# Kernel tuning notes

Measured on AMD Instinct MI355X. Metric: run time of the kernel, lower is better.

Reference implementation:

```python
import jax, jax.numpy as jnp
import numpy as np

# ----- config (mirrors SpatialAxis init) -----
B, N = 1, 32768
D_MODEL, NHEAD, DEPTH = 256, 8, 2
COORD = 3
PATCH = 512          # self.patch_size default
BITS = 10            # self.morton_bits default
SHIFT = True         # self.shift_order default
MLP_H = 4 * D_MODEL
HD = D_MODEL // NHEAD
EPS = 1e-5


def _part1by2(v):
    # spread low 10 bits of int32 so there are 2 zero bits between each
    v = v & 0x000003FF
    v = (v | (v << 16)) & 0x030000FF
    v = (v | (v << 8)) & 0x0300F00F
    v = (v | (v << 4)) & 0x030C30C3
    v = (v | (v << 2)) & 0x09249249
    return v


def _perm_for_block(coords, i):
    # Z-order (Morton) serialization with per-block axis rotation; odd blocks
    # shift the order by half a patch (shifted-window style). Returns [B,N] int32.
    c = jax.lax.stop_gradient(coords)[..., np.roll(np.arange(COORD), -i)]
    cmin = c.min(axis=1, keepdims=True)
    cmax = c.max(axis=1, keepdims=True)
    q = ((c - cmin) / (cmax - cmin + 1e-9) * (2 ** BITS - 1)).astype(jnp.int32)
    q = jnp.clip(q, 0, 2 ** BITS - 1)
    code = (_part1by2(q[..., 0]) | (_part1by2(q[..., 1]) << 1)
            | (_part1by2(q[..., 2]) << 2))  # [B,N]
    perm = jnp.argsort(code, axis=1)
    if SHIFT and (i % 2 == 1):
        perm = jnp.roll(perm, PATCH // 2, axis=1)
    return perm


def _ln(x, g, b):
    m = x.mean(-1, keepdims=True)
    v = x.var(-1, keepdims=True)
    return (x - m) * jax.lax.rsqrt(v + EPS) * g + b


def _point_block(xs, cs, p):
    # xs: [M, P, D] tokens of one patch each; cs: [M, P, 3]
    M, P, D = xs.shape
    h = _ln(xs, p['ln1_g'], p['ln1_b'])
    qkv = h @ p['w_qkv'] + p['b_qkv']                         # [M,P,3D]
    q, k, v = jnp.split(qkv, 3, axis=-1)
    q = q.reshape(M, P, NHEAD, HD)
    k = k.reshape(M, P, NHEAD, HD)
    v = v.reshape(M, P, NHEAD, HD)
    scores = jnp.einsum('mphd,mqhd->mhpq', q, k) / np.sqrt(HD).astype(np.float32)
    rel = cs[:, :, None, :] - cs[:, None, :, :]               # [M,P,P,3]
    bias = jnp.einsum('mpqc,ch->mhpq', rel, p['w_pos']) + p['b_pos'][None, :, None, None]
    attn = jax.nn.softmax(scores + bias, axis=-1)
    o = jnp.einsum('mhpq,mqhd->mphd', attn, v).reshape(M, P, D)
    xs = xs + o @ p['w_proj'] + p['b_proj']
    h2 = _ln(xs, p['ln2_g'], p['ln2_b'])
    xs = xs + jax.nn.gelu(h2 @ p['w_fc1'] + p['b_fc1']) @ p['w_fc2'] + p['b_fc2']
    return xs


def _forward(x, coords, params):
    Cc = coords.shape[-1]
    nblk = N // PATCH
    for i in range(DEPTH):
        p = {k: v[i] for k, v in params.items()}
        perm = _perm_for_block(coords, i)                      # [B,N]
        inv = jnp.argsort(perm, axis=1)
        x_s = jnp.take_along_axis(x, perm[:, :, None], axis=1)
        c_s = jnp.take_along_axis(coords, perm[:, :, None], axis=1)
        x_f = x_s.reshape(B * nblk, PATCH, D_MODEL)
        c_f = c_s.reshape(B * nblk, PATCH, Cc)
        y = _point_block(x_f, c_f, p).reshape(B, N, D_MODEL)
        x = jnp.take_along_axis(y, inv[:, :, None], axis=1)
    return _ln(x, params['norm_g'][0], params['norm_b'][0])


def setup_inputs() -> dict:
    key = jax.random.key(0)
    ks = jax.random.split(key, 20)
    s = 0.02
    d = {
        'x': jax.random.normal(ks[0], (B, N, D_MODEL), jnp.float32),
        'coords': jax.random.uniform(ks[1], (B, N, COORD), jnp.float32),
        'ln1_g': jnp.ones((DEPTH, D_MODEL), jnp.float32),
        'ln1_b': jnp.zeros((DEPTH, D_MODEL), jnp.float32),
        'w_qkv': jax.random.normal(ks[2], (DEPTH, D_MODEL, 3 * D_MODEL), jnp.float32) * s,
        'b_qkv': jnp.zeros((DEPTH, 3 * D_MODEL), jnp.float32),
        'w_proj': jax.random.normal(ks[3], (DEPTH, D_MODEL, D_MODEL), jnp.float32) * s,
        'b_proj': jnp.zeros((DEPTH, D_MODEL), jnp.float32),
        'w_pos': jax.random.normal(ks[4], (DEPTH, COORD, NHEAD), jnp.float32) * s,
        'b_pos': jnp.zeros((DEPTH, NHEAD), jnp.float32),
        'ln2_g': jnp.ones((DEPTH, D_MODEL), jnp.float32),
        'ln2_b': jnp.zeros((DEPTH, D_MODEL), jnp.float32),
        'w_fc1': jax.random.normal(ks[5], (DEPTH, D_MODEL, MLP_H), jnp.float32) * s,
        'b_fc1': jnp.zeros((DEPTH, MLP_H), jnp.float32),
        'w_fc2': jax.random.normal(ks[6], (DEPTH, MLP_H, D_MODEL), jnp.float32) * s,
        'b_fc2': jnp.zeros((DEPTH, D_MODEL), jnp.float32),
        'norm_g': jnp.ones((1, D_MODEL), jnp.float32),
        'norm_b': jnp.zeros((1, D_MODEL), jnp.float32),
    }
    return d


def reference(x, coords, ln1_g, ln1_b, w_qkv, b_qkv, w_proj, b_proj, w_pos, b_pos,
              ln2_g, ln2_b, w_fc1, b_fc1, w_fc2, b_fc2, norm_g, norm_b):
    params = dict(ln1_g=ln1_g, ln1_b=ln1_b, w_qkv=w_qkv, b_qkv=b_qkv,
                  w_proj=w_proj, b_proj=b_proj, w_pos=w_pos, b_pos=b_pos,
                  ln2_g=ln2_g, ln2_b=ln2_b, w_fc1=w_fc1, b_fc1=b_fc1,
                  w_fc2=w_fc2, b_fc2=b_fc2, norm_g=norm_g, norm_b=norm_b)
    return _forward(x, coords, params)
```

## Files before the change

### kernel.cpp

```cpp
#include <hip/hip_runtime.h>

typedef unsigned long long u64;
typedef unsigned int u32;
typedef unsigned short u16;
typedef float f32x4 __attribute__((ext_vector_type(4)));
typedef __bf16 bf16x8 __attribute__((ext_vector_type(8)));

#define N_TOK 32768

__device__ inline u16 f2bf(float f){
  u32 x = __float_as_uint(f);
  u32 r = x + 0x7FFFu + ((x >> 16) & 1u);
  return (u16)(r >> 16);
}

__device__ inline u16 f2bf_hw(float f){
  u32 pk;
  asm("v_cvt_pk_bf16_f32 %0, %1, %2" : "=v"(pk) : "v"(f), "v"(0.f));
  return (u16)pk;
}

__device__ inline f32x4 mfma16(bf16x8 a, bf16x8 b, f32x4 c){
  return __builtin_amdgcn_mfma_f32_16x16x32_bf16(a, b, c, 0, 0, 0);
}

__device__ inline float fexp2(float x){
  float r;
  asm("v_exp_f32 %0, %1" : "=v"(r) : "v"(x));
  return r;
}
__device__ inline float frcp(float x){
  float r;
  asm("v_rcp_f32 %0, %1" : "=v"(r) : "v"(x));
  return r;
}

typedef const __attribute__((address_space(1))) unsigned int* gas_ptr;
typedef __attribute__((address_space(3))) unsigned int* las_ptr;
__device__ inline void gload_lds16(const u16* g, u16* l){
  __builtin_amdgcn_global_load_lds((gas_ptr)g, (las_ptr)l, 16, 0, 0);
}

__device__ inline u32 rp_idx(const u64* __restrict__ keys, int j, int shift){
  return (u32)(keys[(j + N_TOK - shift) & (N_TOK - 1)] & 0xFFFFull);
}

__device__ inline float gelu_tanh(float x){
  float u = 0.7978845608028654f * (x + 0.044715f * x * x * x);
  float e = fexp2(2.8853900817779268f * u);
  return 0.5f * x * (2.0f - 2.0f * frcp(e + 1.0f));
}

__device__ inline u32 part1by2(u32 v){
  v &= 0x3FFu;
  v = (v | (v << 16)) & 0x030000FFu;
  v = (v | (v << 8))  & 0x0300F00Fu;
  v = (v | (v << 4))  & 0x030C30C3u;
  v = (v | (v << 2))  & 0x09249249u;
  return v;
}

__device__ inline void ce64(u64& a, u64& b, bool asc){
  u64 lo = a < b ? a : b;
  u64 hi = a < b ? b : a;
  a = asc ? lo : hi;
  b = asc ? hi : lo;
}

__global__ void minmax_init(u32* __restrict__ cmm){
  int t = threadIdx.x;
  if (t < 3) cmm[t] = 0xFFFFFFFFu;
  else if (t < 6) cmm[t] = 0u;
}

__global__ void __launch_bounds__(256) minmax_atomic(const float* __restrict__ coords,
                                                     u32* __restrict__ cmm){
  __shared__ u32 smn[3], smx[3];
  int t = threadIdx.x;
  if (t < 3){ smn[t] = 0xFFFFFFFFu; smx[t] = 0u; }
  __syncthreads();
  int i = blockIdx.x * 256 + t;
  u32 bits = __float_as_uint(coords[i]);
  int a = i % 3;
  atomicMin(&smn[a], bits);
  atomicMax(&smx[a], bits);
  __syncthreads();
  if (t < 3){
    atomicMin(&cmm[t], smn[t]);
    atomicMax(&cmm[3 + t], smx[t]);
  }
}

__global__ void __launch_bounds__(256) wprep_kernel(const float* __restrict__ src,
                                                    u16* __restrict__ dst, int K, int Nn){
  int layer = blockIdx.y;
  src += (size_t)layer * K * Nn;
  dst += (size_t)layer * K * Nn;
  int ntx = Nn >> 5;
  int tk = blockIdx.x / ntx, tn = blockIdx.x % ntx;
  __shared__ float tile[32][33];
  int r = threadIdx.x >> 5, c = threadIdx.x & 31;
  for (int rr = r; rr < 32; rr += 8)
    tile[rr][c] = src[(size_t)(tk*32 + rr) * Nn + tn*32 + c];
  __syncthreads();
  for (int rr = r; rr < 32; rr += 8)
    dst[(size_t)(tn*32 + rr) * K + tk*32 + c] = f2bf(tile[c][rr]);
}

__global__ void __launch_bounds__(256) codes_kernel(const float* __restrict__ coords,
                                                    const float* __restrict__ cmm,
                                                    u64* __restrict__ keys){
  int p = blockIdx.x * 256 + threadIdx.x;
  int layer = p >> 15, t = p & (N_TOK - 1);
  u32 code = 0;
  #pragma unroll
  for (int j = 0; j < 3; ++j){
    int ax = (j + layer) % 3;
    float c = coords[t*3 + ax];
    float mn = cmm[ax], mx = cmm[3 + ax];
    float v = (c - mn) / (mx - mn + 1e-9f) * 1023.0f;
    int q = (int)v;
    q = q < 0 ? 0 : (q > 1023 ? 1023 : q);
    code |= part1by2((u32)q) << j;
  }
  keys[p] = ((u64)code << 16) | (u32)t;
}

__global__ void __launch_bounds__(64) sort_wave1024(u64* __restrict__ keys){
  int chunk = blockIdx.x;
  int lane = threadIdx.x;
  int base = chunk * 1024 + lane * 16;
  int bl = base & (N_TOK - 1);
  u64 v[16];
  #pragma unroll
  for (int p = 0; p < 16; ++p) v[p] = keys[base + p];
  #pragma unroll
  for (int k2 = 2; k2 <= 16; k2 <<= 1){
    #pragma unroll
    for (int j = k2 >> 1; j > 0; j >>= 1){
      #pragma unroll
      for (int p = 0; p < 16; ++p){
        if ((p & j) == 0){
          bool asc = (((bl + p) & k2) == 0);
          ce64(v[p], v[p+j], asc);
        }
      }
    }
  }
  #pragma unroll
  for (int kk = 32; kk <= 1024; kk <<= 1){
    bool asc = ((bl & kk) == 0);
    #pragma unroll
    for (int j = kk >> 1; j >= 16; j >>= 1){
      int m = j >> 4;
      bool kmin = asc != ((lane & m) != 0);
      #pragma unroll
      for (int p = 0; p < 16; ++p){
        u64 pv = __shfl_xor(v[p], m);
        u64 mn = v[p] < pv ? v[p] : pv;
        u64 mx = v[p] < pv ? pv : v[p];
        v[p] = kmin ? mn : mx;
      }
    }
    #pragma unroll
    for (int j = 8; j > 0; j >>= 1)
      #pragma unroll
      for (int p = 0; p < 16; ++p)
        if ((p & j) == 0) ce64(v[p], v[p+j], asc);
  }
  #pragma unroll
  for (int p = 0; p < 16; ++p) keys[base + p] = v[p];
}

template<int R>
__global__ void __launch_bounds__(256) sort_strided(u64* __restrict__ keys, int logJ, int k){
  const int E = 1 << R;
  int gps = N_TOK >> R;
  int tid = blockIdx.x * 256 + threadIdx.x;
  int seg = tid / gps, gamma = tid % gps;
  int high = gamma >> logJ, low = gamma & ((1 << logJ) - 1);
  int base = seg * N_TOK + (high << (logJ + R)) + low;
  u64 v[E];
  #pragma unroll
  for (int m = 0; m < E; ++m) v[m] = keys[base + (m << logJ)];
  bool asc = (((base & (N_TOK - 1)) & k) == 0);
  #pragma unroll
  for (int jj = R - 1; jj >= 0; --jj)
    #pragma unroll
    for (int m = 0; m < E; ++m)
      if ((m & (1 << jj)) == 0) ce64(v[m], v[m + (1 << jj)], asc);
  #pragma unroll
  for (int m = 0; m < E; ++m) keys[base + (m << logJ)] = v[m];
}

__global__ void __launch_bounds__(64) sort_tail1024(u64* __restrict__ keys, int k){
  int chunk = blockIdx.x;
  int lane = threadIdx.x;
  int base = chunk * 1024 + lane * 16;
  bool asc = ((((chunk * 1024) & (N_TOK - 1)) & k) == 0);
  u64 v[16];
  #pragma unroll
  for (int p = 0; p < 16; ++p) v[p] = keys[base + p];
  #pragma unroll
  for (int m = 32; m >= 1; m >>= 1){
    bool kmin = asc != ((lane & m) != 0);
    #pragma unroll
    for (int p = 0; p < 16; ++p){
      u64 pv = __shfl_xor(v[p], m);
      u64 mn = v[p] < pv ? v[p] : pv;
      u64 mx = v[p] < pv ? pv : v[p];
      v[p] = kmin ? mn : mx;
    }
  }
  #pragma unroll
  for (int j = 8; j > 0; j >>= 1)
    #pragma unroll
    for (int p = 0; p < 16; ++p)
      if ((p & j) == 0) ce64(v[p], v[p+j], asc);
  #pragma unroll
  for (int p = 0; p < 16; ++p) keys[base + p] = v[p];
}

__global__ void __launch_bounds__(256) gather_ln1_kernel(
    const float* __restrict__ xin, const float* __restrict__ coords,
    const u64* __restrict__ keys, int shift,
    const float* __restrict__ g1, const float* __restrict__ b1,
    const float* __restrict__ wpos,
    float* __restrict__ dproj, u16* __restrict__ h){
  int w = threadIdx.x >> 6, lane = threadIdx.x & 63;
  int j = blockIdx.x * 4 + w;
  u32 src = rp_idx(keys, j, shift);
  float4 v = ((const float4*)xin)[(size_t)src * 64 + lane];
  float s = v.x + v.y + v.z + v.w;
  for (int m = 1; m < 64; m <<= 1) s += __shfl_xor(s, m);
  float mean = s * (1.0f / 256.0f);
  float dx = v.x - mean, dy = v.y - mean, dz = v.z - mean, dw = v.w - mean;
  float q = dx*dx + dy*dy + dz*dz + dw*dw;
  for (int m = 1; m < 64; m <<= 1) q += __shfl_xor(q, m);
  float rs = rsqrtf(q * (1.0f / 256.0f) + 1e-5f);
  int c0 = lane * 4;
  u16 h0 = f2bf(dx * rs * g1[c0+0] + b1[c0+0]);
  u16 h1 = f2bf(dy * rs * g1[c0+1] + b1[c0+1]);
  u16 h2 = f2bf(dz * rs * g1[c0+2] + b1[c0+2]);
  u16 h3 = f2bf(dw * rs * g1[c0+3] + b1[c0+3]);
  uint2 pk; pk.x = (u32)h0 | ((u32)h1 << 16); pk.y = (u32)h2 | ((u32)h3 << 16);
  *(uint2*)&h[(size_t)j * 256 + c0] = pk;
  if (lane < 8){
    float acc = 0.0f;
    #pragma unroll
    for (int c = 0; c < 3; ++c) acc += coords[(size_t)src*3 + c] * wpos[c*8 + lane];
    dproj[(size_t)j * 8 + lane] = acc;
  }
}

__global__ void __launch_bounds__(256) ln_bf16_kernel(const float* __restrict__ xin,
    const float* __restrict__ g, const float* __restrict__ b, u16* __restrict__ out){
  int w = threadIdx.x >> 6, lane = threadIdx.x & 63;
  int j = blockIdx.x * 4 + w;
  float4 v = ((const float4*)xin)[(size_t)j * 64 + lane];
  float s = v.x + v.y + v.z + v.w;
  for (int m = 1; m < 64; m <<= 1) s += __shfl_xor(s, m);
  float mean = s * (1.0f / 256.0f);
  float dx = v.x - mean, dy = v.y - mean, dz = v.z - mean, dw = v.w - mean;
  float q = dx*dx + dy*dy + dz*dz + dw*dw;
  for (int m = 1; m < 64; m <<= 1) q += __shfl_xor(q, m);
  float rs = rsqrtf(q * (1.0f / 256.0f) + 1e-5f);
  int c0 = lane * 4;
  u16 h0 = f2bf(dx * rs * g[c0+0] + b[c0+0]);
  u16 h1 = f2bf(dy * rs * g[c0+1] + b[c0+1]);
  u16 h2 = f2bf(dz * rs * g[c0+2] + b[c0+2]);
  u16 h3 = f2bf(dw * rs * g[c0+3] + b[c0+3]);
  uint2 pk; pk.x = (u32)h0 | ((u32)h1 << 16); pk.y = (u32)h2 | ((u32)h3 << 16);
  *(uint2*)&out[(size_t)j * 256 + c0] = pk;
}

__global__ void __launch_bounds__(256) ln_final_kernel(const float* __restrict__ xin,
    const float* __restrict__ g, const float* __restrict__ b, float* __restrict__ out){
  int w = threadIdx.x >> 6, lane = threadIdx.x & 63;
  int j = blockIdx.x * 4 + w;
  float4 v = ((const float4*)xin)[(size_t)j * 64 + lane];
  float s = v.x + v.y + v.z + v.w;
  for (int m = 1; m < 64; m <<= 1) s += __shfl_xor(s, m);
  float mean = s * (1.0f / 256.0f);
  float dx = v.x - mean, dy = v.y - mean, dz = v.z - mean, dw = v.w - mean;
  float q = dx*dx + dy*dy + dz*dz + dw*dw;
  for (int m = 1; m < 64; m <<= 1) q += __shfl_xor(q, m);
  float rs = rsqrtf(q * (1.0f / 256.0f) + 1e-5f);
  int c0 = lane * 4;
  float4 o;
  o.x = dx * rs * g[c0+0] + b[c0+0];
  o.y = dy * rs * g[c0+1] + b[c0+1];
  o.z = dz * rs * g[c0+2] + b[c0+2];
  o.w = dw * rs * g[c0+3] + b[c0+3];
  ((float4*)out)[(size_t)j * 64 + lane] = o;
}

template<int EPI, int BN>
__global__ void __launch_bounds__(1024) gemm2_kernel(
    const u16* __restrict__ A, const u16* __restrict__ Wt,
    const float* __restrict__ bias, int K, int Nn,
    u16* __restrict__ outb, float* __restrict__ outf,
    const float* __restrict__ res, const u64* __restrict__ keys, int shift){
  constexpr int WN = (BN == 256) ? 4 : 2;
  constexpr int WM = 16 / WN;
  constexpr int MI = (256 / WM) / 16;
  constexpr int NI = (BN / WN) / 16;
  constexpr int SPANM = 256 / WM;
  constexpr int SPANN = BN / WN;
  __shared__ __align__(16) u16 As[2][256 * 32];
  __shared__ __align__(16) u16 Bs[2][BN * 32];
  int m0 = blockIdx.x * 256;
  int n0 = blockIdx.y * BN;
  int tid = threadIdx.x;
  int lane = tid & 63, lc = lane & 15, g = lane >> 4;
  int w = tid >> 6;
  int wm = (BN == 256) ? (w >> 2) : (w >> 1);
  int wn = (BN == 256) ? (w & 3) : (w & 1);
  f32x4 acc[MI][NI];
  #pragma unroll
  for (int mi = 0; mi < MI; ++mi)
    #pragma unroll
    for (int ni = 0; ni < NI; ++ni) acc[mi][ni] = (f32x4){0.f,0.f,0.f,0.f};
  int rA = tid >> 2, sA = tid & 3;
  const u16* Ag = A + (size_t)(m0 + rA) * K + (sA ^ ((rA >> 1) & 3)) * 8;
  int cb = (BN == 256) ? tid : (tid & 511);
  int rB = cb >> 2, sB = cb & 3;
  const u16* Bg = Wt + (size_t)(n0 + rB) * K + (sB ^ ((rB >> 1) & 3)) * 8;
  int aofs = (tid & ~63) * 8;
  int bofs = (cb & ~63) * 8;
  int nt = K >> 5;
  auto issue = [&](int t, int b){
    int kk = t << 5;
    gload_lds16(Ag + kk, As[b] + aofs);
    gload_lds16(Bg + kk, Bs[b] + bofs);
  };
  issue(0, 0);
  int cur = 0;
  int fsw = (lc >> 1) & 3;
  for (int t = 0; t < nt; ++t){
    if (t + 1 < nt){
      issue(t + 1, cur ^ 1);
      asm volatile("s_waitcnt vmcnt(2)" ::: "memory");
    } else {
      asm volatile("s_waitcnt vmcnt(0)" ::: "memory");
    }
    __builtin_amdgcn_s_barrier();
    bf16x8 af[MI], bfr[NI];
    #pragma unroll
    for (int mi = 0; mi < MI; ++mi)
      af[mi] = *(const bf16x8*)&As[cur][(wm*SPANM + mi*16 + lc)*32 + (g ^ fsw)*8];
    #pragma unroll
    for (int ni = 0; ni < NI; ++ni)
      bfr[ni] = *(const bf16x8*)&Bs[cur][(wn*SPANN + ni*16 + lc)*32 + (g ^ fsw)*8];
    #pragma unroll
    for (int mi = 0; mi < MI; ++mi)
      #pragma unroll
      for (int ni = 0; ni < NI; ++ni)
        acc[mi][ni] = mfma16(af[mi], bfr[ni], acc[mi][ni]);
    asm volatile("" ::: "memory");
    __builtin_amdgcn_s_barrier();
    cur ^= 1;
  }
  #pragma unroll
  for (int ni = 0; ni < NI; ++ni){
    int col = n0 + wn*SPANN + ni*16 + lc;
    float bv = bias[col];
    #pragma unroll
    for (int mi = 0; mi < MI; ++mi){
      #pragma unroll
      for (int r = 0; r < 4; ++r){
        int row = m0 + wm*SPANM + mi*16 + g*4 + r;
        float v = acc[mi][ni][r] + bv;
        if constexpr (EPI == 0){
          if (col < 256) v *= 0.25500526f;
          outb[(size_t)row * Nn + col] = f2bf_hw(v);
        } else if constexpr (EPI == 1){
          outb[(size_t)row * Nn + col] = f2bf_hw(gelu_tanh(v));
        } else {
          u32 dst = rp_idx(keys, row, shift);
          outf[(size_t)dst * 256 + col] = res[(size_t)row * 256 + col] + v;
        }
      }
    }
  }
}

template<int EPI>
__global__ void __launch_bounds__(256) gemm_kernel(
    const u16* __restrict__ A, const u16* __restrict__ Wt,
    const float* __restrict__ bias, int K, int Nn,
    u16* __restrict__ outb, float* __restrict__ outf,
    const float* __restrict__ res, const u64* __restrict__ keys, int shift){
  __shared__ __align__(16) u16 As[2][128 * 32];
  __shared__ __align__(16) u16 Bs[2][128 * 32];
  int m0 = blockIdx.x * 128;
  int n0 = blockIdx.y * 128;
  int tid = threadIdx.x;
  int lane = tid & 63, lc = lane & 15, g = lane >> 4;
  int w = tid >> 6, wm = w >> 1, wn = w & 1;
  f32x4 acc[4][4];
  #pragma unroll
  for (int mi = 0; mi < 4; ++mi)
    #pragma unroll
    for (int ni = 0; ni < 4; ++ni) acc[mi][ni] = (f32x4){0.f,0.f,0.f,0.f};
  int r1 = tid >> 2, s1 = tid & 3;
  int r2 = r1 + 64;
  int sw = s1 ^ ((r1 >> 1) & 3);
  const u16* Ag1 = A  + (size_t)(m0 + r1) * K + sw*8;
  const u16* Ag2 = A  + (size_t)(m0 + r2) * K + sw*8;
  const u16* Bg1 = Wt + (size_t)(n0 + r1) * K + sw*8;
  const u16* Bg2 = Wt + (size_t)(n0 + r2) * K + sw*8;
  int wofs = (tid & ~63) * 8;
  int nt = K >> 5;
  gload_lds16(Ag1, As[0] + wofs);
  gload_lds16(Ag2, As[0] + wofs + 2048);
  gload_lds16(Bg1, Bs[0] + wofs);
  gload_lds16(Bg2, Bs[0] + wofs + 2048);
  int cur = 0;
  int fsw = (lc >> 1) & 3;
  for (int t = 0; t < nt; ++t){
    if (t + 1 < nt){
      int kk = (t + 1) << 5;
      gload_lds16(Ag1 + kk, As[cur^1] + wofs);
      gload_lds16(Ag2 + kk, As[cur^1] + wofs + 2048);
      gload_lds16(Bg1 + kk, Bs[cur^1] + wofs);
      gload_lds16(Bg2 + kk, Bs[cur^1] + wofs + 2048);
      asm volatile("s_waitcnt vmcnt(4)" ::: "memory");
    } else {
      asm volatile("s_waitcnt vmcnt(0)" ::: "memory");
    }
    __builtin_amdgcn_s_barrier();
    bf16x8 af[4], bfr[4];
    #pragma unroll
    for (int mi = 0; mi < 4; ++mi)
      af[mi] = *(const bf16x8*)&As[cur][(wm*64 + mi*16 + lc)*32 + (g ^ fsw)*8];
    #pragma unroll
    for (int ni = 0; ni < 4; ++ni)
      bfr[ni] = *(const bf16x8*)&Bs[cur][(wn*64 + ni*16 + lc)*32 + (g ^ fsw)*8];
    #pragma unroll
    for (int mi = 0; mi < 4; ++mi)
      #pragma unroll
      for (int ni = 0; ni < 4; ++ni)
        acc[mi][ni] = mfma16(af[mi], bfr[ni], acc[mi][ni]);
    asm volatile("" ::: "memory");
    __builtin_amdgcn_s_barrier();
    cur ^= 1;
  }
  #pragma unroll
  for (int ni = 0; ni < 4; ++ni){
    int col = n0 + wn*64 + ni*16 + lc;
    float bv = bias[col];
    #pragma unroll
    for (int mi = 0; mi < 4; ++mi){
      #pragma unroll
      for (int r = 0; r < 4; ++r){
        int row = m0 + wm*64 + mi*16 + g*4 + r;
        float v = acc[mi][ni][r] + bv;
        if constexpr (EPI == 2){
          u32 src = rp_idx(keys, row, shift);
          outf[(size_t)row * 256 + col] = res[(size_t)src * 256 + col] + v;
        } else {
          outb[(size_t)row * Nn + col] = f2bf_hw(v);
        }
      }
    }
  }
}

#define VSTR 516
#define ATTN_LDS (512*32*2 + 32*VSTR*2 + 512*2)
__global__ void __launch_bounds__(512) attn_kernel(
    const u16* __restrict__ qkvb, const float* __restrict__ dproj,
    u16* __restrict__ o){
  extern __shared__ char smem[];
  u16* Kl = (u16*)smem;
  u16* Vt = (u16*)(smem + 512*32*2);
  u16* wl = (u16*)(smem + 512*32*2 + 32*VSTR*2);
  int h = blockIdx.x & 7;
  int base = (blockIdx.x >> 3) * 512;
  int tid = threadIdx.x, w = tid >> 6, lane = tid & 63, lc = lane & 15, g = lane >> 4;
  const float L2E = 1.4426950408889634f;
  for (int i = tid; i < 2048; i += 512){
    int j = i >> 2, s = i & 3;
    int swc = s ^ ((j >> 1) & 3);
    *(uint4*)&Kl[j*32 + s*8] =
      *(const uint4*)&qkvb[(size_t)(base + j)*768 + 256 + h*32 + swc*8];
  }
  for (int i = tid; i < 1024; i += 512){
    int p = i >> 2, d0 = (i & 3) * 8;
    int j0 = 2*p, j1 = j0 + 1;
    float wv0 = fexp2(-L2E * dproj[(size_t)(base + j0)*8 + h]);
    float wv1 = fexp2(-L2E * dproj[(size_t)(base + j1)*8 + h]);
    uint4 r0 = *(const uint4*)&qkvb[(size_t)(base + j0)*768 + 512 + h*32 + d0];
    uint4 r1 = *(const uint4*)&qkvb[(size_t)(base + j1)*768 + 512 + h*32 + d0];
    const u16* p0 = (const u16*)&r0; const u16* p1 = (const u16*)&r1;
    int j5 = j0 & 31, b = j5 >> 4, m = j5 & 15;
    int slot = (j0 & ~31) + 8*(m >> 2) + 4*b + (m & 3);
    #pragma unroll
    for (int e = 0; e < 8; ++e){
      float f0 = __uint_as_float(((u32)p0[e]) << 16) * wv0;
      float f1 = __uint_as_float(((u32)p1[e]) << 16) * wv1;
      u32 pk;
      asm("v_cvt_pk_bf16_f32 %0, %1, %2" : "=v"(pk) : "v"(f0), "v"(f1));
      *(u32*)&Vt[(d0 + e)*VSTR + slot] = pk;
    }
    if (d0 == 0){
      u32 pkw;
      asm("v_cvt_pk_bf16_f32 %0, %1, %2" : "=v"(pkw) : "v"(wv0), "v"(wv1));
      *(u32*)&wl[slot] = pkw;
    }
  }
  __syncthreads();
  const f32x4 zf = {0.f,0.f,0.f,0.f};
  const bf16x8 zb = {};
  const u16* Qg = qkvb + (size_t)base*768 + h*32;
  int fswk = (lc >> 1) & 3;
  for (int t = 0; t < 4; ++t){
    int q0 = w*64 + t*16;
    bf16x8 qf = *(const bf16x8*)&Qg[(size_t)(q0 + lc)*768 + g*8];
    f32x4 o0 = zf, o1 = zf, lacc = zf;
    #pragma unroll 4
    for (int grp = 0; grp < 16; ++grp){
      int kb = grp * 32;
      bf16x8 kf0 = *(const bf16x8*)&Kl[(kb + lc)*32 + (g ^ fswk)*8];
      bf16x8 kf1 = *(const bf16x8*)&Kl[(kb + 16 + lc)*32 + (g ^ fswk)*8];
      f32x4 s0 = mfma16(kf0, qf, zf);
      f32x4 s1 = mfma16(kf1, qf, zf);
      #pragma unroll
      for (int r = 0; r < 4; ++r){
        s0[r] = fexp2(s0[r]);
        s1[r] = fexp2(s1[r]);
      }
      u32 pk0, pk1, pk2, pk3;
      asm("v_cvt_pk_bf16_f32 %0, %1, %2" : "=v"(pk0) : "v"(s0[0]), "v"(s0[1]));
      asm("v_cvt_pk_bf16_f32 %0, %1, %2" : "=v"(pk1) : "v"(s0[2]), "v"(s0[3]));
      asm("v_cvt_pk_bf16_f32 %0, %1, %2" : "=v"(pk2) : "v"(s1[0]), "v"(s1[1]));
      asm("v_cvt_pk_bf16_f32 %0, %1, %2" : "=v"(pk3) : "v"(s1[2]), "v"(s1[3]));
      bf16x8 pf;
      ((u32*)&pf)[0] = pk0; ((u32*)&pf)[1] = pk1;
      ((u32*)&pf)[2] = pk2; ((u32*)&pf)[3] = pk3;
      bf16x8 v0, v1;
      *(uint2*)&v0       = *(const uint2*)&Vt[lc*VSTR + kb + g*8];
      *((uint2*)&v0 + 1) = *(const uint2*)&Vt[lc*VSTR + kb + g*8 + 4];
      *(uint2*)&v1       = *(const uint2*)&Vt[(16+lc)*VSTR + kb + g*8];
      *((uint2*)&v1 + 1) = *(const uint2*)&Vt[(16+lc)*VSTR + kb + g*8 + 4];
      bf16x8 wf = *(const bf16x8*)&wl[kb + g*8];
      bf16x8 wfz = (lc == 0) ? wf : zb;
      __builtin_amdgcn_s_setprio(1);
      o0 = mfma16(pf, v0, o0);
      o1 = mfma16(pf, v1, o1);
      lacc = mfma16(pf, wfz, lacc);
      __builtin_amdgcn_s_setprio(0);
    }
    #pragma unroll
    for (int r = 0; r < 4; ++r){
      float l = __shfl(lacc[r], lane & 48);
      float inv = 1.0f / l;
      size_t tok = (size_t)(base + q0 + g*4 + r);
      o[tok*256 + h*32 + lc]      = f2bf(o0[r] * inv);
      o[tok*256 + h*32 + 16 + lc] = f2bf(o1[r] * inv);
    }
  }
}

extern "C" void kernel_launch(void* const* d_in, const int* in_sizes, int n_in,
                              void* d_out, int out_size, void* d_ws, size_t ws_size,
                              hipStream_t stream){
  const float* x      = (const float*)d_in[0];
  const float* coords = (const float*)d_in[1];
  const float* ln1_g  = (const float*)d_in[2];
  const float* ln1_b  = (const float*)d_in[3];
  const float* w_qkv  = (const float*)d_in[4];
  const float* b_qkv  = (const float*)d_in[5];
  const float* w_proj = (const float*)d_in[6];
  const float* b_proj = (const float*)d_in[7];
  const float* w_pos  = (const float*)d_in[8];
  const float* ln2_g  = (const float*)d_in[10];
  const float* ln2_b  = (const float*)d_in[11];
  const float* w_fc1  = (const float*)d_in[12];
  const float* b_fc1  = (const float*)d_in[13];
  const float* w_fc2  = (const float*)d_in[14];
  const float* b_fc2  = (const float*)d_in[15];
  const float* norm_g = (const float*)d_in[16];
  const float* norm_b = (const float*)d_in[17];
  float* outp = (float*)d_out;

  hipFuncSetAttribute((const void*)attn_kernel,
                      hipFuncAttributeMaxDynamicSharedMemorySize, ATTN_LDS);

  char* ws = (char*)d_ws;
  size_t off = 0;
  auto alloc = [&](size_t bytes) -> void* {
    void* p = ws + off;
    off += (bytes + 255) & ~(size_t)255;
    return p;
  };
  u64*   keys   = (u64*)  alloc((size_t)2 * N_TOK * 8);
  float* cmm    = (float*)alloc(256);
  float* dproj  = (float*)alloc((size_t)N_TOK * 8 * 4);
  u16*   h      = (u16*)  alloc((size_t)N_TOK * 256 * 2);
  u16*   qkvb   = (u16*)  alloc((size_t)N_TOK * 768 * 2);
  float* x2     = (float*)alloc((size_t)N_TOK * 256 * 4);
  u16*   t      = (u16*)  alloc((size_t)N_TOK * 1024 * 2);
  float* xA     = (float*)alloc((size_t)N_TOK * 256 * 4);
  u16*   wtqkv  = (u16*)  alloc((size_t)2 * 256 * 768 * 2);
  u16*   wtproj = (u16*)  alloc((size_t)2 * 256 * 256 * 2);
  u16*   wtfc1  = (u16*)  alloc((size_t)2 * 256 * 1024 * 2);
  u16*   wtfc2  = (u16*)  alloc((size_t)2 * 1024 * 256 * 2);
  u16*   o      = t;
  float* xB     = (float*)qkvb;
  (void)in_sizes; (void)n_in; (void)out_size; (void)ws_size;

  minmax_init<<<1, 64, 0, stream>>>((u32*)cmm);
  minmax_atomic<<<384, 256, 0, stream>>>(coords, (u32*)cmm);
  wprep_kernel<<<dim3(8*24, 2),  256, 0, stream>>>(w_qkv,  wtqkv,  256, 768);
  wprep_kernel<<<dim3(8*8, 2),   256, 0, stream>>>(w_proj, wtproj, 256, 256);
  wprep_kernel<<<dim3(8*32, 2),  256, 0, stream>>>(w_fc1,  wtfc1,  256, 1024);
  wprep_kernel<<<dim3(32*8, 2),  256, 0, stream>>>(w_fc2,  wtfc2,  1024, 256);

  codes_kernel<<<256, 256, 0, stream>>>(coords, cmm, keys);
  sort_wave1024<<<64, 64, 0, stream>>>(keys);
  sort_strided<1><<<128, 256, 0, stream>>>(keys, 10, 2048);
  sort_tail1024<<<64, 64, 0, stream>>>(keys, 2048);
  sort_strided<2><<<64, 256, 0, stream>>>(keys, 10, 4096);
  sort_tail1024<<<64, 64, 0, stream>>>(keys, 4096);
  sort_strided<3><<<32, 256, 0, stream>>>(keys, 10, 8192);
  sort_tail1024<<<64, 64, 0, stream>>>(keys, 8192);
  sort_strided<3><<<32, 256, 0, stream>>>(keys, 11, 16384);
  sort_strided<1><<<128, 256, 0, stream>>>(keys, 10, 16384);
  sort_tail1024<<<64, 64, 0, stream>>>(keys, 16384);
  sort_strided<3><<<32, 256, 0, stream>>>(keys, 12, 32768);
  sort_strided<2><<<64, 256, 0, stream>>>(keys, 10, 32768);
  sort_tail1024<<<64, 64, 0, stream>>>(keys, 32768);

  for (int layer = 0; layer < 2; ++layer){
    int shift = (layer & 1) ? 256 : 0;
    const float* xin = (layer == 0) ? x : xA;
    float* xout = (layer == 0) ? xA : xB;
    u64* keyL = keys + (size_t)layer * N_TOK;

    gather_ln1_kernel<<<8192, 256, 0, stream>>>(xin, coords, keyL, shift,
        ln1_g + layer*256, ln1_b + layer*256, w_pos + layer*24, dproj, h);
    gemm2_kernel<0,256><<<dim3(128, 3), 1024, 0, stream>>>(h, wtqkv + (size_t)layer*768*256,
        b_qkv + layer*768, 256, 768, qkvb, nullptr, nullptr, nullptr, 0);
    attn_kernel<<<512, 512, ATTN_LDS, stream>>>(qkvb, dproj, o);
    gemm_kernel<2><<<dim3(256, 2), 256, 0, stream>>>(o, wtproj + (size_t)layer*256*256,
        b_proj + layer*256, 256, 256, nullptr, x2, xin, keyL, shift);
    ln_bf16_kernel<<<8192, 256, 0, stream>>>(x2, ln2_g + layer*256, ln2_b + layer*256, h);
    gemm2_kernel<1,256><<<dim3(128, 4), 1024, 0, stream>>>(h, wtfc1 + (size_t)layer*1024*256,
        b_fc1 + layer*1024, 256, 1024, t, nullptr, nullptr, nullptr, 0);
    gemm2_kernel<3,128><<<dim3(128, 2), 1024, 0, stream>>>(t, wtfc2 + (size_t)layer*256*1024,
        b_fc2 + layer*256, 1024, 256, nullptr, xout, x2, keyL, shift);
  }
  ln_final_kernel<<<8192, 256, 0, stream>>>(xB, norm_g, norm_b, outp);
}
```

Measured before the change: 490.2 us.

## Swizzle GEMM blocks across XCDs, merge weight prep, split attention accumulators

The GEMM kernels now use a 1D grid with an XCD-aware block remap, so consecutive M tiles that share A rows land on the same XCD and get better L2 reuse. The four weight-transpose launches are merged into a single launch. In attention, the PV and row-sum MFMA accumulations alternate between two sets of accumulators, which shortens the dependency chain. The row sum now comes from every lane's wf product directly, so the shuffle and the lane-masked weight vector are no longer needed. This adds registers in the attention loop and relies on the grid size being divisible by 8.

```diff
diff --git a/kernel.cpp b/kernel.cpp
--- a/kernel.cpp
+++ b/kernel.cpp
@@ -65,6 +65,11 @@
   u64 hi = a < b ? b : a;
   a = asc ? lo : hi;
   b = asc ? hi : lo;
+}
+
+__device__ inline int xcd_swz(int bid, int nwg){
+  int cpx = nwg >> 3;
+  return (bid & 7) * cpx + (bid >> 3);
 }
 
 __global__ void minmax_init(u32* __restrict__ cmm){
@@ -91,13 +96,23 @@
   }
 }
 
-__global__ void __launch_bounds__(256) wprep_kernel(const float* __restrict__ src,
-                                                    u16* __restrict__ dst, int K, int Nn){
-  int layer = blockIdx.y;
+__global__ void __launch_bounds__(256) wprep_all(
+    const float* __restrict__ w_qkv, const float* __restrict__ w_proj,
+    const float* __restrict__ w_fc1, const float* __restrict__ w_fc2,
+    u16* __restrict__ d_qkv, u16* __restrict__ d_proj,
+    u16* __restrict__ d_fc1, u16* __restrict__ d_fc2){
+  int b = blockIdx.x;
+  const float* src; u16* dst; int K, Nn;
+  if (b < 384){ src = w_qkv; dst = d_qkv; K = 256; Nn = 768; }
+  else if (b < 512){ b -= 384; src = w_proj; dst = d_proj; K = 256; Nn = 256; }
+  else if (b < 1024){ b -= 512; src = w_fc1; dst = d_fc1; K = 256; Nn = 1024; }
+  else { b -= 1024; src = w_fc2; dst = d_fc2; K = 1024; Nn = 256; }
+  int ntx = Nn >> 5;
+  int tpl = (K >> 5) * ntx;
+  int layer = b / tpl, tb = b % tpl;
   src += (size_t)layer * K * Nn;
   dst += (size_t)layer * K * Nn;
-  int ntx = Nn >> 5;
-  int tk = blockIdx.x / ntx, tn = blockIdx.x % ntx;
+  int tk = tb / ntx, tn = tb % ntx;
   __shared__ float tile[32][33];
   int r = threadIdx.x >> 5, c = threadIdx.x & 31;
   for (int rr = r; rr < 32; rr += 8)
@@ -309,8 +324,10 @@
   constexpr int SPANN = BN / WN;
   __shared__ __align__(16) u16 As[2][256 * 32];
   __shared__ __align__(16) u16 Bs[2][BN * 32];
-  int m0 = blockIdx.x * 256;
-  int n0 = blockIdx.y * BN;
+  int swz = xcd_swz(blockIdx.x, gridDim.x);
+  int ntiles = Nn / BN;
+  int m0 = (swz / ntiles) * 256;
+  int n0 = (swz % ntiles) * BN;
   int tid = threadIdx.x;
   int lane = tid & 63, lc = lane & 15, g = lane >> 4;
   int w = tid >> 6;
@@ -393,8 +410,10 @@
     const float* __restrict__ res, const u64* __restrict__ keys, int shift){
   __shared__ __align__(16) u16 As[2][128 * 32];
   __shared__ __align__(16) u16 Bs[2][128 * 32];
-  int m0 = blockIdx.x * 128;
-  int n0 = blockIdx.y * 128;
+  int swz = xcd_swz(blockIdx.x, gridDim.x);
+  int ntiles = Nn / 128;
+  int m0 = (swz / ntiles) * 128;
+  int n0 = (swz % ntiles) * 128;
   int tid = threadIdx.x;
   int lane = tid & 63, lc = lane & 15, g = lane >> 4;
   int w = tid >> 6, wm = w >> 1, wn = w & 1;
@@ -512,13 +531,13 @@
   }
   __syncthreads();
   const f32x4 zf = {0.f,0.f,0.f,0.f};
-  const bf16x8 zb = {};
   const u16* Qg = qkvb + (size_t)base*768 + h*32;
   int fswk = (lc >> 1) & 3;
   for (int t = 0; t < 4; ++t){
     int q0 = w*64 + t*16;
     bf16x8 qf = *(const bf16x8*)&Qg[(size_t)(q0 + lc)*768 + g*8];
-    f32x4 o0 = zf, o1 = zf, lacc = zf;
+    f32x4 oa0 = zf, oa1 = zf, la = zf;
+    f32x4 ob0 = zf, ob1 = zf, lb = zf;
     #pragma unroll 4
     for (int grp = 0; grp < 16; ++grp){
       int kb = grp * 32;
@@ -545,20 +564,24 @@
       *(uint2*)&v1       = *(const uint2*)&Vt[(16+lc)*VSTR + kb + g*8];
       *((uint2*)&v1 + 1) = *(const uint2*)&Vt[(16+lc)*VSTR + kb + g*8 + 4];
       bf16x8 wf = *(const bf16x8*)&wl[kb + g*8];
-      bf16x8 wfz = (lc == 0) ? wf : zb;
       __builtin_amdgcn_s_setprio(1);
-      o0 = mfma16(pf, v0, o0);
-      o1 = mfma16(pf, v1, o1);
-      lacc = mfma16(pf, wfz, lacc);
+      if (grp & 1){
+        ob0 = mfma16(pf, v0, ob0);
+        ob1 = mfma16(pf, v1, ob1);
+        lb  = mfma16(pf, wf, lb);
+      } else {
+        oa0 = mfma16(pf, v0, oa0);
+        oa1 = mfma16(pf, v1, oa1);
+        la  = mfma16(pf, wf, la);
+      }
       __builtin_amdgcn_s_setprio(0);
     }
     #pragma unroll
     for (int r = 0; r < 4; ++r){
-      float l = __shfl(lacc[r], lane & 48);
-      float inv = 1.0f / l;
+      float inv = frcp(la[r] + lb[r]);
       size_t tok = (size_t)(base + q0 + g*4 + r);
-      o[tok*256 + h*32 + lc]      = f2bf(o0[r] * inv);
-      o[tok*256 + h*32 + 16 + lc] = f2bf(o1[r] * inv);
+      o[tok*256 + h*32 + lc]      = f2bf((oa0[r] + ob0[r]) * inv);
+      o[tok*256 + h*32 + 16 + lc] = f2bf((oa1[r] + ob1[r]) * inv);
     }
   }
 }
@@ -613,10 +636,8 @@
 
   minmax_init<<<1, 64, 0, stream>>>((u32*)cmm);
   minmax_atomic<<<384, 256, 0, stream>>>(coords, (u32*)cmm);
-  wprep_kernel<<<dim3(8*24, 2),  256, 0, stream>>>(w_qkv,  wtqkv,  256, 768);
-  wprep_kernel<<<dim3(8*8, 2),   256, 0, stream>>>(w_proj, wtproj, 256, 256);
-  wprep_kernel<<<dim3(8*32, 2),  256, 0, stream>>>(w_fc1,  wtfc1,  256, 1024);
-  wprep_kernel<<<dim3(32*8, 2),  256, 0, stream>>>(w_fc2,  wtfc2,  1024, 256);
+  wprep_all<<<1536, 256, 0, stream>>>(w_qkv, w_proj, w_fc1, w_fc2,
+                                      wtqkv, wtproj, wtfc1, wtfc2);
 
   codes_kernel<<<256, 256, 0, stream>>>(coords, cmm, keys);
   sort_wave1024<<<64, 64, 0, stream>>>(keys);
@@ -641,15 +662,15 @@
 
     gather_ln1_kernel<<<8192, 256, 0, stream>>>(xin, coords, keyL, shift,
         ln1_g + layer*256, ln1_b + layer*256, w_pos + layer*24, dproj, h);
-    gemm2_kernel<0,256><<<dim3(128, 3), 1024, 0, stream>>>(h, wtqkv + (size_t)layer*768*256,
+    gemm2_kernel<0,256><<<384, 1024, 0, stream>>>(h, wtqkv + (size_t)layer*768*256,
         b_qkv + layer*768, 256, 768, qkvb, nullptr, nullptr, nullptr, 0);
     attn_kernel<<<512, 512, ATTN_LDS, stream>>>(qkvb, dproj, o);
-    gemm_kernel<2><<<dim3(256, 2), 256, 0, stream>>>(o, wtproj + (size_t)layer*256*256,
+    gemm_kernel<2><<<512, 256, 0, stream>>>(o, wtproj + (size_t)layer*256*256,
         b_proj + layer*256, 256, 256, nullptr, x2, xin, keyL, shift);
     ln_bf16_kernel<<<8192, 256, 0, stream>>>(x2, ln2_g + layer*256, ln2_b + layer*256, h);
-    gemm2_kernel<1,256><<<dim3(128, 4), 1024, 0, stream>>>(h, wtfc1 + (size_t)layer*1024*256,
+    gemm2_kernel<1,256><<<512, 1024, 0, stream>>>(h, wtfc1 + (size_t)layer*1024*256,
         b_fc1 + layer*1024, 256, 1024, t, nullptr, nullptr, nullptr, 0);
-    gemm2_kernel<3,128><<<dim3(128, 2), 1024, 0, stream>>>(t, wtfc2 + (size_t)layer*256*1024,
+    gemm2_kernel<3,128><<<256, 1024, 0, stream>>>(t, wtfc2 + (size_t)layer*256*1024,
         b_fc2 + layer*256, 1024, 256, nullptr, xout, x2, keyL, shift);
   }
   ln_final_kernel<<<8192, 256, 0, stream>>>(xB, norm_g, norm_b, outp);
```

New measurement: 473.6 us. 3.4% less time.
